# Optimization experiments

Measured on AMD Instinct MI355X. Metric: run time of the kernel, lower is better.

Reference implementation:

```python
import jax, jax.numpy as jnp
import numpy as np

ALPHA = 1.0
BETA = 1.0
B, C, F = 16384, 2000, 1024

def setup_inputs() -> dict:
    key = jax.random.key(0)
    k1, k2, k3, k4 = jax.random.split(key, 4)
    features = jax.random.normal(k1, (B, F), dtype=jnp.float32)
    labels = jax.random.randint(k2, (B,), 0, C, dtype=jnp.int64)
    centers = jax.random.normal(k3, (C, F), dtype=jnp.float32)
    W = jax.random.normal(k4, (C, F), dtype=jnp.float32) * (1.0 / np.sqrt(F))
    b = jnp.zeros((C,), dtype=jnp.float32)
    return {"features": features, "labels": labels, "centers": centers, "W": W, "b": b}

def reference(features, labels, centers, W, b):
    # Fisher (center) loss: only the true-class center distance is used, so
    # gather centers[labels] instead of materializing the [B, C, F] broadcast.
    diff = features - centers[labels]                     # [B, F]
    fisher_loss = jnp.mean(jnp.sum(diff * diff, axis=1))  # scalar
    # Aux cross-entropy over a linear classifier.
    logits = jnp.einsum('bf,cf->bc', features, W) + b     # [B, C]
    logZ = jax.nn.logsumexp(logits, axis=1)               # [B]
    true_logit = jnp.take_along_axis(logits, labels[:, None], axis=1)[:, 0]
    aux_loss = jnp.mean(logZ - true_logit)
    return ALPHA * fisher_loss + BETA * aux_loss
```

## Files before the change

kernel.cpp:

```cpp
#include <hip/hip_runtime.h>
#include <stdint.h>

#define B_ROWS 16384
#define C_CLS  2000
#define C_PAD  2048
#define F_DIM  1024
#define KT     16
#define NRB    64
#define NCBP   16
#define PANEL_A 262144
#define PANEL_BB 131072

typedef float f32x4 __attribute__((ext_vector_type(4)));
typedef long long i64x2 __attribute__((ext_vector_type(2)));

#define SCALE_F 4.0f
#define SCALE_W 16.0f
#define INV_SCALE 0.015625f

__device__ __forceinline__ void gl_lds16(const void* g, void* l) {
    __builtin_amdgcn_global_load_lds(
        (const __attribute__((address_space(1))) unsigned int*)g,
        (__attribute__((address_space(3))) unsigned int*)l, 16, 0, 0);
}

__device__ __forceinline__ unsigned int pk4(float a, float b, float c, float d) {
    int u = __builtin_amdgcn_cvt_pk_fp8_f32(a, b, 0, false);
    u = __builtin_amdgcn_cvt_pk_fp8_f32(c, d, u, true);
    return (unsigned int)u;
}


__global__ __launch_bounds__(256)
void prep_kernel(const float* __restrict__ feat, const int* __restrict__ labels,
                 const float* __restrict__ centers, const float* __restrict__ W,
                 const float* __restrict__ bias,
                 char* __restrict__ A_pre, char* __restrict__ B_pre,
                 float* __restrict__ bias_pad, float* __restrict__ fisher_part)
{
    const int tid = threadIdx.x;
    if (blockIdx.x < 512) {
        const int rt = blockIdx.x >> 2, g = blockIdx.x & 3;
        const int rb = rt >> 1;
        const int r = tid >> 1, h = tid & 1;
        const int grow = rt * 128 + r;
        const int lab = labels[grow];
        const float* frow = feat    + (size_t)grow * F_DIM;
        const float* crow = centers + (size_t)lab  * F_DIM;
        const int frag = (rt & 1) * 8 + (r >> 4);
        char* pan = A_pre + (size_t)rb * PANEL_A + frag * 1024 + (r & 15) * 16;
        float facc = 0.f;
        #pragma unroll
        for (int q = 0; q < 4; ++q) {
            const int kt = g * 4 + q;
            #pragma unroll
            for (int u = 0; u < 2; ++u) {
                const int lhi = h * 2 + u;
                const int k0 = kt * 64 + lhi * 8;
                float4 a0 = *(const float4*)(frow + k0);
                float4 a1 = *(const float4*)(frow + k0 + 4);
                float4 a2 = *(const float4*)(frow + k0 + 32);
                float4 a3 = *(const float4*)(frow + k0 + 36);
                float4 c0 = *(const float4*)(crow + k0);
                float4 c1 = *(const float4*)(crow + k0 + 4);
                float4 c2 = *(const float4*)(crow + k0 + 32);
                float4 c3 = *(const float4*)(crow + k0 + 36);
                float d0 = a0.x-c0.x, d1 = a0.y-c0.y, d2 = a0.z-c0.z, d3 = a0.w-c0.w;
                float d4 = a1.x-c1.x, d5 = a1.y-c1.y, d6 = a1.z-c1.z, d7 = a1.w-c1.w;
                facc += d0*d0 + d1*d1 + d2*d2 + d3*d3 + d4*d4 + d5*d5 + d6*d6 + d7*d7;
                d0 = a2.x-c2.x; d1 = a2.y-c2.y; d2 = a2.z-c2.z; d3 = a2.w-c2.w;
                d4 = a3.x-c3.x; d5 = a3.y-c3.y; d6 = a3.z-c3.z; d7 = a3.w-c3.w;
                facc += d0*d0 + d1*d1 + d2*d2 + d3*d3 + d4*d4 + d5*d5 + d6*d6 + d7*d7;
                uint4 o = { pk4(SCALE_F*a0.x, SCALE_F*a0.y, SCALE_F*a0.z, SCALE_F*a0.w),
                            pk4(SCALE_F*a1.x, SCALE_F*a1.y, SCALE_F*a1.z, SCALE_F*a1.w),
                            pk4(SCALE_F*a2.x, SCALE_F*a2.y, SCALE_F*a2.z, SCALE_F*a2.w),
                            pk4(SCALE_F*a3.x, SCALE_F*a3.y, SCALE_F*a3.z, SCALE_F*a3.w) };
                *(uint4*)(pan + kt * 16384 + lhi * 256) = o;
            }
        }
        for (int d = 32; d >= 1; d >>= 1) facc += __shfl_xor(facc, d);
        __shared__ float redw[4];
        const int wid = tid >> 6, lane = tid & 63;
        if (lane == 0) redw[wid] = facc;
        __syncthreads();
        if (tid == 0) fisher_part[blockIdx.x] = redw[0] + redw[1] + redw[2] + redw[3];
    } else {
        const int b = blockIdx.x - 512;
        const int ct = b >> 3, ktg = b & 7;
        const int rcol = tid >> 1, h = tid & 1;
        const int gc = ct * 128 + rcol;
        char* pan = B_pre + (size_t)ct * PANEL_BB + (rcol >> 4) * 1024 + (rcol & 15) * 16;
        #pragma unroll
        for (int q = 0; q < 2; ++q) {
            const int kt = ktg * 2 + q;
            #pragma unroll
            for (int u = 0; u < 2; ++u) {
                const int lhi = h * 2 + u;
                uint4 o;
                if (gc < C_CLS) {
                    const float* src = W + (size_t)gc * F_DIM + kt * 64 + lhi * 8;
                    float4 a0 = *(const float4*)(src);
                    float4 a1 = *(const float4*)(src + 4);
                    float4 a2 = *(const float4*)(src + 32);
                    float4 a3 = *(const float4*)(src + 36);
                    o = (uint4){ pk4(SCALE_W*a0.x, SCALE_W*a0.y, SCALE_W*a0.z, SCALE_W*a0.w),
                                 pk4(SCALE_W*a1.x, SCALE_W*a1.y, SCALE_W*a1.z, SCALE_W*a1.w),
                                 pk4(SCALE_W*a2.x, SCALE_W*a2.y, SCALE_W*a2.z, SCALE_W*a2.w),
                                 pk4(SCALE_W*a3.x, SCALE_W*a3.y, SCALE_W*a3.z, SCALE_W*a3.w) };
                } else {
                    o = (uint4){0u, 0u, 0u, 0u};
                }
                *(uint4*)(pan + kt * 8192 + lhi * 256) = o;
            }
        }
        if (b < C_PAD / 256) {
            const int i = b * 256 + tid;
            bias_pad[i] = (i < C_CLS) ? bias[i] : -1e30f;
        }
    }
}

__global__ __launch_bounds__(256, 2)
void gemm_kernel(const int* __restrict__ labels, const float* __restrict__ biasp,
                 const char* __restrict__ A_pre, const char* __restrict__ B_pre,
                 float* __restrict__ s_part, float* __restrict__ tl_part)
{
    __shared__ alignas(128) char smem[32768];

    const int cpx = gridDim.x >> 3;
    const int wg = (blockIdx.x & 7) * cpx + (blockIdx.x >> 3);
    const int cb = wg & 15;
    const int rb = wg >> 4;

    const int tid = threadIdx.x;
    const int w = tid >> 6, lane = tid & 63;
    const int l15 = lane & 15, lhi = lane >> 4;

    const char* Apan = A_pre + (size_t)rb * PANEL_A + w * 4096 + lane * 16;
    const char* Bsrc = B_pre + (size_t)cb * PANEL_BB;

    f32x4 acc[4][8];
    #pragma unroll
    for (int mi = 0; mi < 4; ++mi)
        #pragma unroll
        for (int ni = 0; ni < 8; ++ni) acc[mi][ni] = (f32x4){0.f, 0.f, 0.f, 0.f};

    i64x2 aE[4], aO[4], bE[8], bO[8];

#define LOADA(SA, KTT) do {                                                           \
    const char* pa_ = Apan + (KTT) * 16384;                                           \
    _Pragma("unroll")                                                                 \
    for (int i_ = 0; i_ < 4; ++i_) SA[i_] = *(const i64x2*)(pa_ + i_ * 1024);         \
} while (0)

#define STAGEB(KTT) do {                                                              \
    const char* sb_ = Bsrc + (size_t)(KTT) * 8192 + w * 2048 + lane * 16;             \
    char* db_ = smem + ((KTT) & 3) * 8192 + w * 2048;                                 \
    gl_lds16(sb_, db_);                                                               \
    gl_lds16(sb_ + 1024, db_ + 1024);                                                 \
} while (0)

#define READB(SB, KTT) do {                                                           \
    const char* lb_ = smem + ((KTT) & 3) * 8192 + lane * 16;                          \
    _Pragma("unroll")                                                                 \
    for (int i_ = 0; i_ < 8; ++i_) SB[i_] = *(const i64x2*)(lb_ + i_ * 1024);         \
} while (0)

#define MFMA64(SA, SB) do {                                                           \
    __builtin_amdgcn_s_setprio(1);                                                    \
    _Pragma("unroll")                                                                 \
    for (int kf_ = 0; kf_ < 2; ++kf_)                                                 \
        _Pragma("unroll")                                                             \
        for (int mi_ = 0; mi_ < 4; ++mi_)                                             \
            _Pragma("unroll")                                                         \
            for (int ni_ = 0; ni_ < 8; ++ni_)                                         \
                acc[mi_][ni_] = __builtin_amdgcn_mfma_f32_16x16x32_fp8_fp8(           \
                    SA[mi_][kf_], SB[ni_][kf_], acc[mi_][ni_], 0, 0, 0);              \
    __builtin_amdgcn_s_setprio(0);                                                    \
} while (0)

#define FENCE __builtin_amdgcn_sched_barrier(0)
#define WAITV(N) asm volatile("s_waitcnt vmcnt(" #N ")" ::: "memory")
#define BAR __builtin_amdgcn_s_barrier()

    STAGEB(0);
    STAGEB(1);
    LOADA(aE, 0);
    WAITV(6);
    FENCE; BAR; FENCE;
    READB(bE, 0);

    #pragma unroll 1
    for (int k2 = 0; k2 < 7; ++k2) {
        STAGEB(2 * k2 + 2);
        LOADA(aO, 2 * k2 + 1);
        FENCE;
        WAITV(10);
        FENCE; BAR; FENCE;
        READB(bO, 2 * k2 + 1);
        FENCE;
        MFMA64(aE, bE);
        FENCE;
        STAGEB(2 * k2 + 3);
        LOADA(aE, 2 * k2 + 2);
        FENCE;
        WAITV(10);
        FENCE; BAR; FENCE;
        READB(bE, 2 * k2 + 2);
        FENCE;
        MFMA64(aO, bO);
        FENCE;
    }
    LOADA(aO, 15);
    FENCE;
    WAITV(8);
    FENCE; BAR; FENCE;
    READB(bO, 15);
    FENCE;
    MFMA64(aE, bE);
    FENCE;
    MFMA64(aO, bO);

#undef LOADA
#undef STAGEB
#undef READB
#undef MFMA64
#undef FENCE
#undef WAITV
#undef BAR

    float bb[8];
    #pragma unroll
    for (int ni = 0; ni < 8; ++ni)
        bb[ni] = biasp[cb * 128 + ni * 16 + l15];

    #pragma unroll
    for (int mi = 0; mi < 4; ++mi) {
        #pragma unroll
        for (int j = 0; j < 4; ++j) {
            const int rl = w * 64 + mi * 16 + lhi * 4 + j;
            const int lab = labels[rb * 256 + rl];
            float sv = 0.f, tv = 0.f;
            #pragma unroll
            for (int ni = 0; ni < 8; ++ni) {
                const float v = fmaf(acc[mi][ni][j], INV_SCALE, bb[ni]);
                sv += __expf(v);
                const int gc = cb * 128 + ni * 16 + l15;
                tv = (gc == lab) ? v : tv;
            }
            #pragma unroll
            for (int d = 1; d < 16; d <<= 1) {
                sv += __shfl_xor(sv, d);
                tv += __shfl_xor(tv, d);
            }
            if (l15 == 0) {
                const int grow = rb * 256 + rl;
                s_part[(size_t)cb * B_ROWS + grow]  = sv;
                tl_part[(size_t)cb * B_ROWS + grow] = tv;
            }
        }
    }
}

__global__ __launch_bounds__(256)
void rowcomb_kernel(const float* __restrict__ s_part, const float* __restrict__ tl_part,
                    float* __restrict__ aux_part)
{
    const int row = blockIdx.x * 256 + threadIdx.x;
    float s = 0.f, t = 0.f;
    #pragma unroll
    for (int p = 0; p < NCBP; ++p) {
        s += s_part[(size_t)p * B_ROWS + row];
        t += tl_part[(size_t)p * B_ROWS + row];
    }
    float acc = __logf(s) - t;
    for (int d = 32; d >= 1; d >>= 1) acc += __shfl_xor(acc, d);
    __shared__ float red[4];
    const int wid = threadIdx.x >> 6, lane = threadIdx.x & 63;
    if (lane == 0) red[wid] = acc;
    __syncthreads();
    if (threadIdx.x == 0) aux_part[blockIdx.x] = red[0] + red[1] + red[2] + red[3];
}

__global__ __launch_bounds__(256)
void final_kernel(const float* __restrict__ fisher_part, const float* __restrict__ aux_part,
                  float* __restrict__ out)
{
    const int tid = threadIdx.x;
    float acc = fisher_part[tid] + fisher_part[256 + tid];
    if (tid < 64) acc += aux_part[tid];
    for (int d = 32; d >= 1; d >>= 1) acc += __shfl_xor(acc, d);
    __shared__ float red[4];
    const int wid = tid >> 6, lane = tid & 63;
    if (lane == 0) red[wid] = acc;
    __syncthreads();
    if (tid == 0) out[0] = (red[0] + red[1] + red[2] + red[3]) * (1.0f / (float)B_ROWS);
}

extern "C" void kernel_launch(void* const* d_in, const int* in_sizes, int n_in,
                              void* d_out, int out_size, void* d_ws, size_t ws_size,
                              hipStream_t stream)
{
    (void)in_sizes; (void)n_in; (void)out_size; (void)ws_size;
    const float* feat    = (const float*)d_in[0];
    const int*   labels  = (const int*)  d_in[1];
    const float* centers = (const float*)d_in[2];
    const float* W       = (const float*)d_in[3];
    const float* bias    = (const float*)d_in[4];
    float* out = (float*)d_out;
    char* ws = (char*)d_ws;

    const size_t szA    = (size_t)NRB  * PANEL_A;
    const size_t szB    = (size_t)NCBP * PANEL_BB;
    const size_t szBias = (size_t)C_PAD * 4;

    char* A_pre = ws;
    char* B_pre = ws + szA;
    float* bias_pad    = (float*)(ws + szA + szB);
    float* s_part      = (float*)(ws + szA + szB + szBias);
    float* tl_part     = s_part + (size_t)NCBP * B_ROWS;
    float* fisher_part = tl_part + (size_t)NCBP * B_ROWS;
    float* aux_part    = fisher_part + 512;

    prep_kernel<<<640, 256, 0, stream>>>(feat, labels, centers, W, bias,
                                         A_pre, B_pre, bias_pad, fisher_part);
    gemm_kernel<<<NRB * NCBP, 256, 0, stream>>>(labels, bias_pad, A_pre, B_pre, s_part, tl_part);
    rowcomb_kernel<<<B_ROWS / 256, 256, 0, stream>>>(s_part, tl_part, aux_part);
    final_kernel<<<1, 256, 0, stream>>>(fisher_part, aux_part, out);
}
```

Measured before the change: 84.65 us.

## Deepen B-tile LDS ring to eight stages and barrier once per four k-tiles

Doubles the shared-memory ring for the B operand from four to eight 8KB slots and prefetches four k-tiles ahead. Each group of four k-tiles is then consumed with a single vmcnt wait and workgroup barrier, instead of one wait and barrier per k-tile. The goal is to cut synchronisation stalls and hide global-load latency behind more MFMA work. In exchange, each block uses 64KB of LDS, which could limit occupancy.

```diff
diff --git a/kernel.cpp b/kernel.cpp
--- a/kernel.cpp
+++ b/kernel.cpp
@@ -125,7 +125,7 @@
                  const char* __restrict__ A_pre, const char* __restrict__ B_pre,
                  float* __restrict__ s_part, float* __restrict__ tl_part)
 {
-    __shared__ alignas(128) char smem[32768];
+    __shared__ alignas(128) char smem[65536];
 
     const int cpx = gridDim.x >> 3;
     const int wg = (blockIdx.x & 7) * cpx + (blockIdx.x >> 3);
@@ -155,13 +155,13 @@
 
 #define STAGEB(KTT) do {                                                              \
     const char* sb_ = Bsrc + (size_t)(KTT) * 8192 + w * 2048 + lane * 16;             \
-    char* db_ = smem + ((KTT) & 3) * 8192 + w * 2048;                                 \
+    char* db_ = smem + ((KTT) & 7) * 8192 + w * 2048;                                 \
     gl_lds16(sb_, db_);                                                               \
     gl_lds16(sb_ + 1024, db_ + 1024);                                                 \
 } while (0)
 
 #define READB(SB, KTT) do {                                                           \
-    const char* lb_ = smem + ((KTT) & 3) * 8192 + lane * 16;                          \
+    const char* lb_ = smem + ((KTT) & 7) * 8192 + lane * 16;                          \
     _Pragma("unroll")                                                                 \
     for (int i_ = 0; i_ < 8; ++i_) SB[i_] = *(const i64x2*)(lb_ + i_ * 1024);         \
 } while (0)
@@ -183,43 +183,49 @@
 #define WAITV(N) asm volatile("s_waitcnt vmcnt(" #N ")" ::: "memory")
 #define BAR __builtin_amdgcn_s_barrier()
 
-    STAGEB(0);
-    STAGEB(1);
+    STAGEB(0); STAGEB(1); STAGEB(2); STAGEB(3);
     LOADA(aE, 0);
-    WAITV(6);
+    WAITV(4);
     FENCE; BAR; FENCE;
     READB(bE, 0);
+    FENCE;
 
     #pragma unroll 1
-    for (int k2 = 0; k2 < 7; ++k2) {
-        STAGEB(2 * k2 + 2);
-        LOADA(aO, 2 * k2 + 1);
-        FENCE;
-        WAITV(10);
-        FENCE; BAR; FENCE;
-        READB(bO, 2 * k2 + 1);
+    for (int g = 0; g < 4; ++g) {
+        const int k0 = g * 4;
+        const bool st = (g < 3);
+        if (st) STAGEB(k0 + 4);
+        LOADA(aO, k0 + 1);
+        READB(bO, k0 + 1);
         FENCE;
         MFMA64(aE, bE);
         FENCE;
-        STAGEB(2 * k2 + 3);
-        LOADA(aE, 2 * k2 + 2);
-        FENCE;
-        WAITV(10);
-        FENCE; BAR; FENCE;
-        READB(bE, 2 * k2 + 2);
+        if (st) STAGEB(k0 + 5);
+        LOADA(aE, k0 + 2);
+        READB(bE, k0 + 2);
         FENCE;
         MFMA64(aO, bO);
         FENCE;
+        if (st) STAGEB(k0 + 6);
+        LOADA(aO, k0 + 3);
+        READB(bO, k0 + 3);
+        FENCE;
+        MFMA64(aE, bE);
+        FENCE;
+        if (st) {
+            STAGEB(k0 + 7);
+            LOADA(aE, k0 + 4);
+        }
+        FENCE;
+        MFMA64(aO, bO);
+        FENCE;
+        if (st) {
+            WAITV(4);
+            FENCE; BAR; FENCE;
+            READB(bE, k0 + 4);
+            FENCE;
+        }
     }
-    LOADA(aO, 15);
-    FENCE;
-    WAITV(8);
-    FENCE; BAR; FENCE;
-    READB(bO, 15);
-    FENCE;
-    MFMA64(aE, bE);
-    FENCE;
-    MFMA64(aO, bO);
 
 #undef LOADA
 #undef STAGEB
```

New measurement: 184.0 us. 2.17x slower.
